# Kernel optimization log

Measured on AMD Instinct MI355X. Metric: run time of the kernel, lower is better.

Reference implementation:

```python
import jax, jax.numpy as jnp
import numpy as np

B, BEAM, TMAX, V, D, H, NL, S, DFF = 4, 5, 16, 50257, 768, 12, 2, 128, 3072
BUF = TMAX + 1  # prefix buffer: sos + TMAX generated tokens
DH = D // H
SOS, EOS = 1, 2
NEG = -1e20


def _ln(x, g, b):
    m = x.mean(-1, keepdims=True)
    v = ((x - m) ** 2).mean(-1, keepdims=True)
    return (x - m) / jnp.sqrt(v + 1e-5) * g + b


def _mha(q_in, kv_in, in_w, in_b, out_w, out_b, bias=None, kpm=None):
    # PyTorch-style MHA: packed in_proj [3D, D], out_proj [D, D]
    q = q_in @ in_w[:D].T + in_b[:D]
    k = kv_in @ in_w[D:2 * D].T + in_b[D:2 * D]
    v = kv_in @ in_w[2 * D:].T + in_b[2 * D:]
    Bq, Tq = q.shape[0], q.shape[1]
    Tk = k.shape[1]
    q = q.reshape(Bq, Tq, H, DH)
    k = k.reshape(Bq, Tk, H, DH)
    v = v.reshape(Bq, Tk, H, DH)
    s = jnp.einsum('bqhd,bkhd->bhqk', q, k) * (1.0 / np.sqrt(DH))
    if bias is not None:
        s = s + bias  # additive causal bias (-10000 * (1 - tril)), as in source
    if kpm is not None:
        s = jnp.where(kpm[:, None, None, :], -1e9, s)  # memory_key_padding_mask
    a = jax.nn.softmax(s, axis=-1)
    o = jnp.einsum('bhqk,bkhd->bqhd', a, v).reshape(Bq, Tq, D)
    return o @ out_w.T + out_b


def _decode(emb, pos, ln_emb_g, ln_emb_b, self_in_w, self_in_b, self_out_w,
            self_out_b, cross_in_w, cross_in_b, cross_out_w, cross_out_b,
            ff1_w, ff1_b, ff2_w, ff2_b, ln1_g, ln1_b, ln2_g, ln2_b, ln3_g,
            ln3_b, dense_w, dense_b, context, source_mask):
    causal = -10000.0 * (1.0 - jnp.tril(jnp.ones((BUF, BUF), jnp.float32)))
    mem = jnp.repeat(context, BEAM, axis=0)            # [B*BEAM, S, D]
    kpm = jnp.repeat(source_mask == 0, BEAM, axis=0)   # True = pad
    # Beam init: nextYs[0] = [sos, 0, 0, ...]; scores trick makes step-0 pick
    # from beam row 0 only, matching beamLk = wordLk[0] in the source.
    buf0 = jnp.zeros((B, BEAM, BUF), jnp.int32).at[:, 0, 0].set(SOS)
    s0 = jnp.concatenate([jnp.zeros((1,), jnp.float32),
                          jnp.full((BEAM - 1,), NEG, jnp.float32)])
    scores0 = jnp.broadcast_to(s0, (B, BEAM))

    def step(carry, t):
        scores, buf = carry
        # no KV cache: re-run full decoder each step (fixed-size padded buffer;
        # causal mask makes positions <= t identical to running on the prefix)
        x = emb[buf.reshape(B * BEAM, BUF)] + pos[None, :BUF]
        x = _ln(x, ln_emb_g, ln_emb_b)
        for l in range(NL):  # post-norm TransformerDecoderLayer, dropout=eval
            sa = _mha(x, x, self_in_w[l], self_in_b[l], self_out_w[l],
                      self_out_b[l], bias=causal)
            x = _ln(x + sa, ln1_g[l], ln1_b[l])
            ca = _mha(x, mem, cross_in_w[l], cross_in_b[l], cross_out_w[l],
                      cross_out_b[l], kpm=kpm)
            x = _ln(x + ca, ln2_g[l], ln2_b[l])
            ff = jax.nn.relu(x @ ff1_w[l].T + ff1_b[l]) @ ff2_w[l].T + ff2_b[l]
            x = _ln(x + ff, ln3_g[l], ln3_b[l])
        h = jnp.tanh(jnp.take(x, t, axis=1) @ dense_w.T + dense_b)  # last pos
        logp = jax.nn.log_softmax(h @ emb.T, axis=-1).reshape(B, BEAM, V)
        last = jnp.take(buf, t, axis=2)  # previous token per beam
        beamLk = logp + scores[:, :, None]
        beamLk = jnp.where((last == EOS)[:, :, None], NEG, beamLk)
        vals, ids = jax.lax.top_k(beamLk.reshape(B, BEAM * V), BEAM)
        prevK = ids // V
        tok = (ids % V).astype(jnp.int32)
        buf = jnp.take_along_axis(buf, prevK[:, :, None], axis=1)
        buf = buf.at[:, :, t + 1].set(tok)
        return (vals, buf), None

    (scores, buf), _ = jax.lax.scan(step, (scores0, buf0), jnp.arange(TMAX))
    toks = buf[:, :, 1:]                         # backtracked hypotheses
    keep = jnp.cumsum(toks == EOS, axis=-1) == 0  # truncate at eos, pad with 0
    preds = jnp.where(keep, toks, 0)
    return scores, preds


def setup_inputs() -> dict:
    key = jax.random.key(0)
    ks = jax.random.split(key, 12)
    r = lambda k, shape: jax.random.normal(k, shape, jnp.float32) * 0.02
    inp = {}
    inp['emb'] = r(ks[0], (V, D))
    inp['pos'] = r(ks[1], (BUF, D))
    inp['ln_emb_g'] = jnp.ones((D,), jnp.float32)
    inp['ln_emb_b'] = jnp.zeros((D,), jnp.float32)
    inp['self_in_w'] = r(ks[2], (NL, 3 * D, D))
    inp['self_in_b'] = jnp.zeros((NL, 3 * D), jnp.float32)
    inp['self_out_w'] = r(ks[3], (NL, D, D))
    inp['self_out_b'] = jnp.zeros((NL, D), jnp.float32)
    inp['cross_in_w'] = r(ks[4], (NL, 3 * D, D))
    inp['cross_in_b'] = jnp.zeros((NL, 3 * D), jnp.float32)
    inp['cross_out_w'] = r(ks[5], (NL, D, D))
    inp['cross_out_b'] = jnp.zeros((NL, D), jnp.float32)
    inp['ff1_w'] = r(ks[6], (NL, DFF, D))
    inp['ff1_b'] = jnp.zeros((NL, DFF), jnp.float32)
    inp['ff2_w'] = r(ks[7], (NL, D, DFF))
    inp['ff2_b'] = jnp.zeros((NL, D), jnp.float32)
    inp['ln1_g'] = jnp.ones((NL, D), jnp.float32)
    inp['ln1_b'] = jnp.zeros((NL, D), jnp.float32)
    inp['ln2_g'] = jnp.ones((NL, D), jnp.float32)
    inp['ln2_b'] = jnp.zeros((NL, D), jnp.float32)
    inp['ln3_g'] = jnp.ones((NL, D), jnp.float32)
    inp['ln3_b'] = jnp.zeros((NL, D), jnp.float32)
    inp['dense_w'] = r(ks[8], (D, D))
    inp['dense_b'] = jnp.zeros((D,), jnp.float32)
    inp['context'] = jax.random.normal(ks[9], (B, S, D), jnp.float32)
    inp['source_mask'] = jnp.ones((B, S), jnp.int32)
    return inp


def reference(emb, pos, ln_emb_g, ln_emb_b, self_in_w, self_in_b, self_out_w,
              self_out_b, cross_in_w, cross_in_b, cross_out_w, cross_out_b,
              ff1_w, ff1_b, ff2_w, ff2_b, ln1_g, ln1_b, ln2_g, ln2_b, ln3_g,
              ln3_b, dense_w, dense_b, context, source_mask):
    return _decode(emb, pos, ln_emb_g, ln_emb_b, self_in_w, self_in_b,
                   self_out_w, self_out_b, cross_in_w, cross_in_b,
                   cross_out_w, cross_out_b, ff1_w, ff1_b, ff2_w, ff2_b,
                   ln1_g, ln1_b, ln2_g, ln2_b, ln3_g, ln3_b, dense_w,
                   dense_b, context, source_mask)
```

## Files before the change

### kernel.cpp

```cpp
#include <hip/hip_runtime.h>
#include <cfloat>
#include <cmath>

constexpr int kV   = 50257;
constexpr int kVP  = 50432;
constexpr int kD   = 768;
constexpr int NLY  = 2;
constexpr int BB   = 4;
constexpr int BEAM = 5;
constexpr int RR   = BB * BEAM;
constexpr int BUFL = 17;
constexpr int SS   = 128;
constexpr int DFF  = 3072;
constexpr int TMAX = 16;
constexpr int SOS  = 1;
constexpr int EOSt = 2;
constexpr int LB   = (kV + 255) / 256;
#define NEGV (-1e20f)

__device__ inline float wave_sum(float v) {
#pragma unroll
  for (int o = 32; o > 0; o >>= 1) v += __shfl_xor(v, o, 64);
  return v;
}
__device__ inline float wave_max(float v) {
#pragma unroll
  for (int o = 32; o > 0; o >>= 1) v = fmaxf(v, __shfl_xor(v, o, 64));
  return v;
}
__device__ inline bool better(float v1, int i1, float v2, int i2) {
  return v1 > v2 || (v1 == v2 && i1 < i2);
}
__device__ inline void insert5(float* tv, int* ti, float v, int i) {
  if (better(v, i, tv[4], ti[4])) {
    tv[4] = v; ti[4] = i;
#pragma unroll
    for (int s = 4; s > 0; --s)
      if (better(tv[s], ti[s], tv[s - 1], ti[s - 1])) {
        float fv = tv[s]; tv[s] = tv[s - 1]; tv[s - 1] = fv;
        int iv = ti[s]; ti[s] = ti[s - 1]; ti[s - 1] = iv;
      }
  }
}
__device__ inline float sel5f(const float* a, int i) {
  float r = a[0];
  r = (i == 1) ? a[1] : r; r = (i == 2) ? a[2] : r;
  r = (i == 3) ? a[3] : r; r = (i == 4) ? a[4] : r;
  return r;
}
__device__ inline int sel5i(const int* a, int i) {
  int r = a[0];
  r = (i == 1) ? a[1] : r; r = (i == 2) ? a[2] : r;
  r = (i == 3) ? a[3] : r; r = (i == 4) ? a[4] : r;
  return r;
}
__device__ inline void merge5(float* av, int* ai, const float* bv, const int* bi) {
  float cv[5]; int ci[5];
  int ia = 0, ib = 0;
#pragma unroll
  for (int s = 0; s < 5; ++s) {
    float va = sel5f(av, ia); int xa = sel5i(ai, ia);
    float vb = sel5f(bv, ib); int xb = sel5i(bi, ib);
    bool ta = better(va, xa, vb, xb);
    cv[s] = ta ? va : vb; ci[s] = ta ? xa : xb;
    ia += ta ? 1 : 0; ib += ta ? 0 : 1;
  }
#pragma unroll
  for (int s = 0; s < 5; ++s) { av[s] = cv[s]; ai[s] = ci[s]; }
}

__global__ void init_k(int* buf0, float* scores) {
  int tid = threadIdx.x;
  if (tid < RR * BUFL) buf0[tid] = 0;
  __syncthreads();
  if (tid < BB) buf0[tid * BEAM * BUFL] = SOS;
  if (tid < RR) scores[tid] = (tid % BEAM == 0) ? 0.f : NEGV;
}

__global__ void transpose_k(const float* __restrict__ src, float* __restrict__ dst,
                            int R, int C, int ds) {
  __shared__ float tile[32][33];
  const int c0 = blockIdx.x * 32, r0 = blockIdx.y * 32;
  const int lx = threadIdx.x & 31, ly = threadIdx.x >> 5;
#pragma unroll
  for (int j = 0; j < 4; ++j) {
    int r = r0 + ly + j * 8;
    if (r < R && c0 + lx < C) tile[ly + j * 8][lx] = src[(size_t)r * C + c0 + lx];
  }
  __syncthreads();
#pragma unroll
  for (int j = 0; j < 4; ++j) {
    int c = c0 + ly + j * 8;
    if (c < C && r0 + lx < R) dst[(size_t)c * ds + r0 + lx] = tile[lx][ly + j * 8];
  }
}

template<bool WT>
__global__ __launch_bounds__(256) void crosskv_k(
    const float* __restrict__ ctx, const float* __restrict__ Wm0,
    const float* __restrict__ bias0, float* __restrict__ ck, float* __restrict__ cv) {
  const int l = blockIdx.z;
  const float* Wm = Wm0 + (size_t)l * 2304 * 768;
  const float* bias = bias0 + l * 2304;
  __shared__ float a_s[16 * 768];
  __shared__ float ps[4 * 64 * 17];
  const int tid = threadIdx.x;
  const int row0 = blockIdx.y * 16;
  for (int i = tid * 4; i < 16 * 768; i += 1024) {
    int rr = i / 768, k = i - rr * 768;
    *(float4*)&a_s[i] = *(const float4*)&ctx[(size_t)(row0 + rr) * 768 + k];
  }
  __syncthreads();
  const int w = tid >> 6, lane = tid & 63;
  const int colg = 768 + blockIdx.x * 64 + lane;
  const int kb = w * 192;
  float acc[16];
#pragma unroll
  for (int r = 0; r < 16; ++r) acc[r] = 0.f;
  for (int k4 = 0; k4 < 48; ++k4) {
    const int k = kb + k4 * 4;
    float w0, w1, w2, w3;
    if (WT) {
      w0 = Wm[(size_t)(k + 0) * 2304 + colg]; w1 = Wm[(size_t)(k + 1) * 2304 + colg];
      w2 = Wm[(size_t)(k + 2) * 2304 + colg]; w3 = Wm[(size_t)(k + 3) * 2304 + colg];
    } else {
      float4 wv = *(const float4*)&Wm[(size_t)colg * 768 + k];
      w0 = wv.x; w1 = wv.y; w2 = wv.z; w3 = wv.w;
    }
#pragma unroll
    for (int r = 0; r < 16; ++r) {
      float4 a = *(const float4*)&a_s[r * 768 + k];
      acc[r] = fmaf(a.x, w0, fmaf(a.y, w1, fmaf(a.z, w2, fmaf(a.w, w3, acc[r]))));
    }
  }
#pragma unroll
  for (int r = 0; r < 16; ++r) ps[(w * 64 + lane) * 17 + r] = acc[r];
  __syncthreads();
  for (int o = tid; o < 1024; o += 256) {
    int rr = o >> 6, cl = o & 63;
    int cg = 768 + blockIdx.x * 64 + cl;
    float v = bias[cg];
#pragma unroll
    for (int ww = 0; ww < 4; ++ww) v += ps[(ww * 64 + cl) * 17 + rr];
    int gr = row0 + rr;
    int b = gr >> 7, s = gr & 127;
    int c = cg - 768, kv = c / 768, n = c - kv * 768;
    float* dst = kv ? cv : ck;
    dst[((size_t)(l * 4 + b) * 128 + s) * 768 + n] = v;
  }
}

template<bool WT>
__global__ __launch_bounds__(256) void gemm20_k(
    const float* __restrict__ Wm, int wstride, const float* __restrict__ bias, int N,
    int pre, const float* __restrict__ xsrc, const float* __restrict__ tmp_in,
    const float* __restrict__ lng, const float* __restrict__ lnb, float* __restrict__ xout,
    int outmode, float* __restrict__ out0,
    float* __restrict__ kcl, float* __restrict__ vcl, int t,
    const float* __restrict__ embp, const float* __restrict__ posw, const int* __restrict__ bufn,
    int reorder_t, const float* __restrict__ kco, const float* __restrict__ vco,
    float* __restrict__ kcn, float* __restrict__ vcn, const int* __restrict__ prevK) {
  __shared__ float a_s[RR * 768];
  __shared__ float ps[4 * 64 * 21];
  __shared__ float mS[RR], rS[RR];
  __shared__ int tokS[RR];
  const int tid = threadIdx.x;

  if (reorder_t > 0) {
    const int per = 768 * reorder_t;
    const int tot = 2 * RR * per;
    for (int i = blockIdx.x * 256 + tid; i < tot; i += gridDim.x * 256) {
      int half = i / (RR * per);
      int rem = i - half * RR * per;
      int r = rem / per;
      int rem2 = rem - r * per;
      int p = rem2 / 768;
      int d = rem2 - p * 768;
      int src = (r / BEAM) * BEAM + prevK[r];
      if (half == 0) kcn[(r * BUFL + p) * 768 + d] = kco[(src * BUFL + p) * 768 + d];
      else           vcn[(r * BUFL + p) * 768 + d] = vco[(src * BUFL + p) * 768 + d];
    }
  }
  if (pre == 1 && tid < RR) tokS[tid] = bufn[tid * BUFL + t];
  __syncthreads();
  for (int i = tid * 4; i < RR * 768; i += 1024) {
    int r = i / 768, k = i - r * 768;
    float4 v;
    if (pre == 0) v = *(const float4*)&xsrc[i];
    else if (pre == 1) {
      float4 e = *(const float4*)&embp[(size_t)tokS[r] * 768 + k];
      float4 p = *(const float4*)&posw[(size_t)t * 768 + k];
      v = make_float4(e.x + p.x, e.y + p.y, e.z + p.z, e.w + p.w);
    } else {
      float4 a = *(const float4*)&xsrc[i];
      float4 b = *(const float4*)&tmp_in[i];
      v = make_float4(a.x + b.x, a.y + b.y, a.z + b.z, a.w + b.w);
    }
    *(float4*)&a_s[i] = v;
  }
  __syncthreads();
  if (pre != 0) {
    const int w0 = tid >> 6, ln = tid & 63;
    for (int r = w0 * 5; r < w0 * 5 + 5; ++r) {
      float s = 0.f, q = 0.f;
      for (int k = ln; k < 768; k += 64) { float v = a_s[r * 768 + k]; s += v; q += v * v; }
      s = wave_sum(s); q = wave_sum(q);
      if (ln == 0) {
        float m = s / 768.f;
        float var = q / 768.f - m * m;
        mS[r] = m; rS[r] = 1.f / sqrtf(var + 1e-5f);
      }
    }
    __syncthreads();
    for (int i = tid * 4; i < RR * 768; i += 1024) {
      int r = i / 768, k = i - r * 768;
      float4 v = *(const float4*)&a_s[i];
      float4 g = *(const float4*)&lng[k];
      float4 b = *(const float4*)&lnb[k];
      float m = mS[r], rs = rS[r];
      v = make_float4((v.x - m) * rs * g.x + b.x, (v.y - m) * rs * g.y + b.y,
                      (v.z - m) * rs * g.z + b.z, (v.w - m) * rs * g.w + b.w);
      *(float4*)&a_s[i] = v;
    }
    __syncthreads();
    if (xout != nullptr && blockIdx.x == 0) {
      for (int i = tid * 4; i < RR * 768; i += 1024)
        *(float4*)&xout[i] = *(const float4*)&a_s[i];
    }
  }
  const int w = tid >> 6, lane = tid & 63;
  const int colg = blockIdx.x * 64 + lane;
  const int kb = w * 192;
  float acc[RR];
#pragma unroll
  for (int r = 0; r < RR; ++r) acc[r] = 0.f;
  for (int k4 = 0; k4 < 48; ++k4) {
    const int k = kb + k4 * 4;
    float w0, w1, w2, w3;
    if (WT) {
      w0 = Wm[(size_t)(k + 0) * wstride + colg]; w1 = Wm[(size_t)(k + 1) * wstride + colg];
      w2 = Wm[(size_t)(k + 2) * wstride + colg]; w3 = Wm[(size_t)(k + 3) * wstride + colg];
    } else {
      float4 wv = *(const float4*)&Wm[(size_t)colg * 768 + k];
      w0 = wv.x; w1 = wv.y; w2 = wv.z; w3 = wv.w;
    }
#pragma unroll
    for (int r = 0; r < RR; ++r) {
      float4 a = *(const float4*)&a_s[r * 768 + k];
      acc[r] = fmaf(a.x, w0, fmaf(a.y, w1, fmaf(a.z, w2, fmaf(a.w, w3, acc[r]))));
    }
  }
#pragma unroll
  for (int r = 0; r < RR; ++r) ps[(w * 64 + lane) * 21 + r] = acc[r];
  __syncthreads();
  for (int o = tid; o < RR * 64; o += 256) {
    int r = o >> 6, cl = o & 63;
    int cg = blockIdx.x * 64 + cl;
    float v = bias[cg];
#pragma unroll
    for (int ww = 0; ww < 4; ++ww) v += ps[(ww * 64 + cl) * 21 + r];
    if (outmode == 1) v = fmaxf(v, 0.f);
    else if (outmode == 2) v = tanhf(v);
    if (outmode == 3) {
      if (cg < 768) out0[r * 768 + cg];
      if (cg < 768) out0[r * 768 + cg] = v;
      else if (cg < 1536) kcl[(r * BUFL + t) * 768 + (cg - 768)] = v;
      else vcl[(r * BUFL + t) * 768 + (cg - 1536)] = v;
    } else {
      out0[(size_t)r * N + cg] = v;
    }
  }
}

template<bool WT>
__global__ __launch_bounds__(1024) void ff2_k(
    const float* __restrict__ Wm, const float* __restrict__ bias,
    const float* __restrict__ A, float* __restrict__ out0) {
  __shared__ float ps[64 * 16 * 21];
  const int tid = threadIdx.x;
  const int w = tid >> 6, lane = tid & 63;
  const int cl = lane & 15, ksub = lane >> 4;
  const int colg = blockIdx.x * 16 + cl;
  const int kb = w * 192 + ksub * 48;
  float acc[RR];
#pragma unroll
  for (int r = 0; r < RR; ++r) acc[r] = 0.f;
  for (int k4 = 0; k4 < 12; ++k4) {
    const int k = kb + k4 * 4;
    float w0, w1, w2, w3;
    if (WT) {
      w0 = Wm[(size_t)(k + 0) * 768 + colg]; w1 = Wm[(size_t)(k + 1) * 768 + colg];
      w2 = Wm[(size_t)(k + 2) * 768 + colg]; w3 = Wm[(size_t)(k + 3) * 768 + colg];
    } else {
      float4 wv = *(const float4*)&Wm[(size_t)colg * 3072 + k];
      w0 = wv.x; w1 = wv.y; w2 = wv.z; w3 = wv.w;
    }
#pragma unroll
    for (int r = 0; r < RR; ++r) {
      float4 a = *(const float4*)&A[r * 3072 + k];
      acc[r] = fmaf(a.x, w0, fmaf(a.y, w1, fmaf(a.z, w2, fmaf(a.w, w3, acc[r]))));
    }
  }
  const int seg = w * 4 + ksub;
#pragma unroll
  for (int r = 0; r < RR; ++r) ps[(seg * 16 + cl) * 21 + r] = acc[r];
  __syncthreads();
  if (tid < RR * 16) {
    int r = tid >> 4, c2 = tid & 15;
    float v = bias[blockIdx.x * 16 + c2];
    for (int s2 = 0; s2 < 64; ++s2) v += ps[(s2 * 16 + c2) * 21 + r];
    out0[r * 768 + blockIdx.x * 16 + c2] = v;
  }
}

__global__ __launch_bounds__(64) void self_attn_k(
    const float* __restrict__ qb, const float* __restrict__ kcn,
    const float* __restrict__ vcn, float* __restrict__ outb, int t) {
  const int r = blockIdx.x, hh = blockIdx.y, lane = threadIdx.x;
  __shared__ float qs[64];
  __shared__ float ks[16 * 65];
  __shared__ float pp[16];
  qs[lane] = qb[r * 768 + hh * 64 + lane];
  for (int p = 0; p <= t; ++p)
    ks[p * 65 + lane] = kcn[(r * BUFL + p) * 768 + hh * 64 + lane];
  __syncthreads();
  float s = -1e30f;
  if (lane <= t) {
    float a = 0.f;
#pragma unroll
    for (int d = 0; d < 64; ++d) a = fmaf(qs[d], ks[lane * 65 + d], a);
    s = a * 0.125f;
  }
  float m = wave_max(s);
  float p = expf(s - m);
  float sum = wave_sum(p);
  if (lane <= t) pp[lane] = p / sum;
  __syncthreads();
  const float* vb = vcn + r * BUFL * 768 + hh * 64 + lane;
  float o = 0.f;
  for (int k = 0; k <= t; ++k) o = fmaf(pp[k], vb[k * 768], o);
  outb[r * 768 + hh * 64 + lane] = o;
}

__global__ __launch_bounds__(64) void cross_attn_k(
    const float* __restrict__ qb, const float* __restrict__ ck,
    const float* __restrict__ cv, const int* __restrict__ smask,
    float* __restrict__ outb) {
  const int r = blockIdx.x, hh = blockIdx.y, lane = threadIdx.x;
  const int b = r / BEAM;
  __shared__ float qs[64];
  __shared__ float ks[128 * 65];
  __shared__ float pp[128];
  qs[lane] = qb[r * 768 + hh * 64 + lane];
  for (int p = 0; p < 128; ++p)
    ks[p * 65 + lane] = ck[((size_t)b * 128 + p) * 768 + hh * 64 + lane];
  __syncthreads();
  float a0 = 0.f, a1 = 0.f;
#pragma unroll
  for (int d = 0; d < 64; ++d) {
    a0 = fmaf(qs[d], ks[lane * 65 + d], a0);
    a1 = fmaf(qs[d], ks[(lane + 64) * 65 + d], a1);
  }
  float s0 = a0 * 0.125f, s1 = a1 * 0.125f;
  if (smask[b * 128 + lane] == 0)      s0 = -1e9f;
  if (smask[b * 128 + lane + 64] == 0) s1 = -1e9f;
  float m = wave_max(fmaxf(s0, s1));
  float p0 = expf(s0 - m), p1 = expf(s1 - m);
  float sum = wave_sum(p0 + p1);
  pp[lane] = p0 / sum; pp[lane + 64] = p1 / sum;
  __syncthreads();
  const float* vb = cv + (size_t)b * 128 * 768 + hh * 64 + lane;
  float o0 = 0.f, o1 = 0.f, o2 = 0.f, o3 = 0.f;
  for (int k = 0; k < 128; k += 4) {
    o0 = fmaf(pp[k + 0], vb[(k + 0) * 768], o0);
    o1 = fmaf(pp[k + 1], vb[(k + 1) * 768], o1);
    o2 = fmaf(pp[k + 2], vb[(k + 2) * 768], o2);
    o3 = fmaf(pp[k + 3], vb[(k + 3) * 768], o3);
  }
  outb[r * 768 + hh * 64 + lane] = (o0 + o1) + (o2 + o3);
}

template<bool ET>
__global__ __launch_bounds__(256) void logits_k(
    const float* __restrict__ hbuf, const float* __restrict__ embM,
    float* __restrict__ candV, int* __restrict__ candI,
    float* __restrict__ mrow, float* __restrict__ srow) {
  __shared__ float hs[RR * 768];
  __shared__ float vv[4 * 256];
  const int tid = threadIdx.x, blk = blockIdx.x;
  for (int i = tid * 4; i < RR * 768; i += 1024)
    *(float4*)&hs[i] = *(const float4*)&hbuf[i];
  __syncthreads();
  const int col = blk * 256 + tid;
  const bool valid = col < kV;
  const int colc = valid ? col : (kV - 1);
  float acc[RR];
#pragma unroll
  for (int r = 0; r < RR; ++r) acc[r] = 0.f;
  for (int k = 0; k < 768; k += 4) {
    float w0, w1, w2, w3;
    if (ET) {
      w0 = embM[(size_t)(k + 0) * kVP + col]; w1 = embM[(size_t)(k + 1) * kVP + col];
      w2 = embM[(size_t)(k + 2) * kVP + col]; w3 = embM[(size_t)(k + 3) * kVP + col];
    } else {
      float4 wv = *(const float4*)&embM[(size_t)colc * 768 + k];
      w0 = wv.x; w1 = wv.y; w2 = wv.z; w3 = wv.w;
    }
#pragma unroll
    for (int r = 0; r < RR; ++r) {
      float4 a = *(const float4*)&hs[r * 768 + k];
      acc[r] = fmaf(a.x, w0, fmaf(a.y, w1, fmaf(a.z, w2, fmaf(a.w, w3, acc[r]))));
    }
  }
  const int w = tid >> 6, lane = tid & 63;
  for (int g = 0; g < 5; ++g) {
#pragma unroll
    for (int j = 0; j < 4; ++j) vv[j * 256 + tid] = valid ? acc[g * 4 + j] : -FLT_MAX;
    __syncthreads();
    const int r = g * 4 + w;
    float v[4]; int gc[4]; bool used[4];
#pragma unroll
    for (int j = 0; j < 4; ++j) {
      v[j] = vv[w * 256 + lane * 4 + j];
      gc[j] = blk * 256 + lane * 4 + j;
      used[j] = false;
    }
    float tv[5]; int tg[5];
#pragma unroll
    for (int round = 0; round < 5; ++round) {
      float bv = -FLT_MAX; int bidx = 0x7fffffff; int bj = -1;
#pragma unroll
      for (int j = 0; j < 4; ++j) {
        bool c = (!used[j]) && better(v[j], gc[j], bv, bidx);
        bv = c ? v[j] : bv; bidx = c ? gc[j] : bidx; bj = c ? j : bj;
      }
      float wv2 = bv; int wi = bidx;
      for (int d = 1; d < 64; d <<= 1) {
        float ov = __shfl_xor(wv2, d, 64); int oi = __shfl_xor(wi, d, 64);
        if (better(ov, oi, wv2, wi)) { wv2 = ov; wi = oi; }
      }
      tv[round] = wv2; tg[round] = wi;
      if (bj >= 0 && bidx == wi) used[bj] = true;
    }
    float m = tv[0];
    float s = 0.f;
#pragma unroll
    for (int j = 0; j < 4; ++j) s += expf(v[j] - m);
    s = wave_sum(s);
    if (lane == 0) {
      mrow[r * LB + blk] = m;
      srow[r * LB + blk] = s;
#pragma unroll
      for (int q = 0; q < 5; ++q) {
        candV[(r * LB + blk) * 5 + q] = tv[q];
        candI[(r * LB + blk) * 5 + q] = tg[q];
      }
    }
    __syncthreads();
  }
}

__global__ __launch_bounds__(256) void topk_k(
    const float* __restrict__ candV, const int* __restrict__ candI,
    const float* __restrict__ mrow, const float* __restrict__ srow,
    float* __restrict__ scores, const int* __restrict__ bufc, int* __restrict__ bufn,
    int t, int* __restrict__ prevK, int* __restrict__ tokv) {
  const int b = blockIdx.x, tid = threadIdx.x;
  const int w = tid >> 6, lane = tid & 63;
  __shared__ float lseS[5], scS[5];
  __shared__ int emS[5];
  __shared__ float wv5[4][5]; __shared__ int wi5[4][5];
  __shared__ int fpk[5], ftok[5];
  for (int j = w; j < 5; j += 4) {
    const int gr = b * 5 + j;
    float M = -FLT_MAX, S = 0.f;
    for (int e = lane; e < LB; e += 64) {
      float m2 = mrow[gr * LB + e], s2 = srow[gr * LB + e];
      if (m2 > M) { S = S * expf(M - m2) + s2; M = m2; }
      else        { S += s2 * expf(m2 - M); }
    }
    for (int d = 1; d < 64; d <<= 1) {
      float Mo = __shfl_xor(M, d, 64), So = __shfl_xor(S, d, 64);
      float Mn = fmaxf(M, Mo);
      S = S * expf(M - Mn) + So * expf(Mo - Mn);
      M = Mn;
    }
    if (lane == 0) {
      lseS[j] = M + logf(S);
      scS[j] = scores[gr];
      emS[j] = (bufc[gr * BUFL + t] == EOSt);
    }
  }
  __syncthreads();
  float tv[5]; int ti[5];
#pragma unroll
  for (int s = 0; s < 5; ++s) { tv[s] = -FLT_MAX; ti[s] = 0x7fffffff; }
  for (int i = tid; i < 5 * LB * 5; i += 256) {
    int j = i / (LB * 5);
    int e = i - j * LB * 5;
    int blk = e / 5, rk = e - blk * 5;
    int gr = b * 5 + j;
    float cvv = candV[(gr * LB + blk) * 5 + rk];
    int col = candI[(gr * LB + blk) * 5 + rk];
    float val = emS[j] ? NEGV : (cvv - lseS[j] + scS[j]);
    insert5(tv, ti, val, j * kV + col);
  }
  for (int d = 1; d < 64; d <<= 1) {
    float ov[5]; int oi[5];
#pragma unroll
    for (int s = 0; s < 5; ++s) { ov[s] = __shfl_xor(tv[s], d, 64); oi[s] = __shfl_xor(ti[s], d, 64); }
    merge5(tv, ti, ov, oi);
  }
  if (lane == 0) {
#pragma unroll
    for (int s = 0; s < 5; ++s) { wv5[w][s] = tv[s]; wi5[w][s] = ti[s]; }
  }
  __syncthreads();
  if (tid == 0) {
    float av[5]; int ai[5];
#pragma unroll
    for (int s = 0; s < 5; ++s) { av[s] = wv5[0][s]; ai[s] = wi5[0][s]; }
    for (int ww = 1; ww < 4; ++ww) {
      float bv[5]; int bi[5];
#pragma unroll
      for (int s = 0; s < 5; ++s) { bv[s] = wv5[ww][s]; bi[s] = wi5[ww][s]; }
      merge5(av, ai, bv, bi);
    }
#pragma unroll
    for (int s = 0; s < 5; ++s) {
      int pk = ai[s] / kV;
      int tk = ai[s] - pk * kV;
      scores[b * 5 + s] = av[s];
      prevK[b * 5 + s] = pk; tokv[b * 5 + s] = tk;
      fpk[s] = pk; ftok[s] = tk;
    }
  }
  __syncthreads();
  for (int i = tid; i < 5 * BUFL; i += 256) {
    int j = i / BUFL, p = i - j * BUFL;
    int src = b * 5 + fpk[j];
    int val = (p == t + 1) ? ftok[j] : bufc[src * BUFL + p];
    bufn[(b * 5 + j) * BUFL + p] = val;
  }
}

__global__ void finalize_k(const float* __restrict__ scores, const int* __restrict__ buf,
                           float* __restrict__ out) {
  const int tid = threadIdx.x;
  if (tid < RR) {
    out[tid] = scores[tid];
    int seen = 0;
    for (int i = 0; i < TMAX; ++i) {
      int tk = buf[tid * BUFL + 1 + i];
      if (tk == EOSt) seen = 1;
      out[RR + tid * TMAX + i] = seen ? 0.f : (float)tk;
    }
  }
}

extern "C" void kernel_launch(void* const* d_in, const int* in_sizes, int n_in,
                              void* d_out, int out_size, void* d_ws, size_t ws_size,
                              hipStream_t stream) {
  const float* emb        = (const float*)d_in[0];
  const float* pos        = (const float*)d_in[1];
  const float* ln_emb_g   = (const float*)d_in[2];
  const float* ln_emb_b   = (const float*)d_in[3];
  const float* self_in_w  = (const float*)d_in[4];
  const float* self_in_b  = (const float*)d_in[5];
  const float* self_out_w = (const float*)d_in[6];
  const float* self_out_b = (const float*)d_in[7];
  const float* cross_in_w = (const float*)d_in[8];
  const float* cross_in_b = (const float*)d_in[9];
  const float* cross_out_w= (const float*)d_in[10];
  const float* cross_out_b= (const float*)d_in[11];
  const float* ff1_w      = (const float*)d_in[12];
  const float* ff1_b      = (const float*)d_in[13];
  const float* ff2_w      = (const float*)d_in[14];
  const float* ff2_b      = (const float*)d_in[15];
  const float* ln1_g      = (const float*)d_in[16];
  const float* ln1_b      = (const float*)d_in[17];
  const float* ln2_g      = (const float*)d_in[18];
  const float* ln2_b      = (const float*)d_in[19];
  const float* ln3_g      = (const float*)d_in[20];
  const float* ln3_b      = (const float*)d_in[21];
  const float* dense_w    = (const float*)d_in[22];
  const float* dense_b    = (const float*)d_in[23];
  const float* context    = (const float*)d_in[24];
  const int*   source_mask= (const int*)d_in[25];

  float* wsf = (float*)d_ws;
  size_t off = 0;
  auto alloc = [&](size_t n) { float* p = wsf + off; off += (n + 3) & ~(size_t)3; return p; };

  float* XA    = alloc(RR * 768);
  float* XB    = alloc(RR * 768);
  float* XC    = alloc(RR * 768);
  float* qb    = alloc(RR * 768);
  float* attnb = alloc(RR * 768);
  float* tmp   = alloc(RR * 768);
  float* hbuf  = alloc(RR * 768);
  float* ffb   = alloc(RR * 3072);
  float* candV = alloc(RR * LB * 5);
  float* mrow  = alloc(RR * LB);
  float* srow  = alloc(RR * LB);
  float* scores= alloc(32);
  float* ck    = alloc((size_t)NLY * 4 * 128 * 768);
  float* cv    = alloc((size_t)NLY * 4 * 128 * 768);
  const size_t cacheSeg = (size_t)RR * BUFL * 768;
  float* kcB   = alloc(4 * cacheSeg);
  float* vcB   = alloc(4 * cacheSeg);
  int* candI   = (int*)alloc(RR * LB * 5);
  int* bufs0   = (int*)alloc(RR * BUFL + 12);
  int* bufs1   = (int*)alloc(RR * BUFL + 12);
  int* prevKp  = (int*)alloc(32);
  int* tokp    = (int*)alloc(32);
  const size_t baseFloats = off;

  const size_t nSiT = (size_t)768 * 2304, nSoT = (size_t)768 * 768;
  const size_t nCiT = nSiT, nCoT = nSoT, nF1T = (size_t)768 * 3072, nF2T = (size_t)3072 * 768;
  const size_t wtFloats = 2 * (nSiT + nSoT + nCiT + nCoT + nF1T + nF2T) + nSoT;
  const size_t embTFloats = (size_t)768 * kVP;
  const bool useWT = ws_size >= (baseFloats + wtFloats) * 4;
  const bool useET = useWT && ws_size >= (baseFloats + wtFloats + embTFloats) * 4;

  float* siT[2]; float* soT[2]; float* ciT[2]; float* coT[2]; float* f1T[2]; float* f2T[2];
  float* dT = nullptr; float* embT = nullptr;
  if (useWT) {
    for (int l = 0; l < 2; ++l) siT[l] = alloc(nSiT);
    for (int l = 0; l < 2; ++l) soT[l] = alloc(nSoT);
    for (int l = 0; l < 2; ++l) ciT[l] = alloc(nCiT);
    for (int l = 0; l < 2; ++l) coT[l] = alloc(nCoT);
    for (int l = 0; l < 2; ++l) f1T[l] = alloc(nF1T);
    for (int l = 0; l < 2; ++l) f2T[l] = alloc(nF2T);
    dT = alloc(nSoT);
    if (useET) embT = alloc(embTFloats);
  }

  init_k<<<1, 512, 0, stream>>>(bufs0, scores);

  if (useWT) {
    auto T = [&](const float* src, float* dst, int R, int C, int ds) {
      dim3 g((C + 31) / 32, (R + 31) / 32);
      transpose_k<<<g, 256, 0, stream>>>(src, dst, R, C, ds);
    };
    for (int l = 0; l < 2; ++l) {
      T(self_in_w  + (size_t)l * 2304 * 768, siT[l], 2304, 768, 2304);
      T(self_out_w + (size_t)l * 768 * 768,  soT[l], 768, 768, 768);
      T(cross_in_w + (size_t)l * 2304 * 768, ciT[l], 2304, 768, 2304);
      T(cross_out_w+ (size_t)l * 768 * 768,  coT[l], 768, 768, 768);
      T(ff1_w      + (size_t)l * 3072 * 768, f1T[l], 3072, 768, 3072);
      T(ff2_w      + (size_t)l * 768 * 3072, f2T[l], 768, 3072, 768);
    }
    T(dense_w, dT, 768, 768, 768);
    if (useET) T(emb, embT, kV, 768, kVP);
  }

  {
    dim3 g(24, 32, 2);
    if (useWT) crosskv_k<true><<<g, 256, 0, stream>>>(context, ciT[0], cross_in_b, ck, cv);
    else       crosskv_k<false><<<g, 256, 0, stream>>>(context, cross_in_w, cross_in_b, ck, cv);
  }

  const int* bc = bufs0;
  auto G = [&](const float* Wt, const float* Wg, int wstride,
               const float* bias, int N, int pre, const float* xsrc, const float* tmpin,
               const float* g2, const float* b2, float* xout, int outmode, float* out0,
               float* kcl, float* vcl, int tt,
               int reorder_t, const float* kco, const float* vco, float* kcn2, float* vcn2) {
    dim3 grid(N / 64);
    if (useWT)
      gemm20_k<true><<<grid, 256, 0, stream>>>(Wt, wstride, bias, N, pre, xsrc, tmpin, g2, b2,
        xout, outmode, out0, kcl, vcl, tt, emb, pos, bc, reorder_t, kco, vco, kcn2, vcn2, prevKp);
    else
      gemm20_k<false><<<grid, 256, 0, stream>>>(Wg, wstride, bias, N, pre, xsrc, tmpin, g2, b2,
        xout, outmode, out0, kcl, vcl, tt, emb, pos, bc, reorder_t, kco, vco, kcn2, vcn2, prevKp);
  };

  for (int t = 0; t < TMAX; ++t) {
    bc = (t & 1) ? bufs1 : bufs0;
    int* bn = (t & 1) ? bufs0 : bufs1;
    const int np = (t + 1) & 1, op = t & 1;

    for (int l = 0; l < 2; ++l) {
      float* kNew = kcB + (np * 2 + l) * cacheSeg;
      float* vNew = vcB + (np * 2 + l) * cacheSeg;
      float* kOld = kcB + (op * 2 + l) * cacheSeg;
      float* vOld = vcB + (op * 2 + l) * cacheSeg;
      if (l == 0)
        G(siT[0], self_in_w, 2304, self_in_b, 2304,
          1, nullptr, nullptr, ln_emb_g, ln_emb_b, XA,
          3, qb, kNew, vNew, t, t, kOld, vOld, kNew, vNew);
      else
        G(siT[1], self_in_w + (size_t)2304 * 768, 2304, self_in_b + 2304, 2304,
          2, XC, tmp, ln3_g, ln3_b, XA,
          3, qb, kNew, vNew, t, t, kOld, vOld, kNew, vNew);
      self_attn_k<<<dim3(RR, 12), 64, 0, stream>>>(qb, kNew, vNew, attnb, t);
      G(soT[l], self_out_w + (size_t)l * 768 * 768, 768, self_out_b + l * 768, 768,
        0, attnb, nullptr, nullptr, nullptr, nullptr, 0, tmp,
        nullptr, nullptr, t, 0, nullptr, nullptr, nullptr, nullptr);
      G(ciT[l], cross_in_w + (size_t)l * 2304 * 768, 2304, cross_in_b + l * 2304, 768,
        2, XA, tmp, ln1_g + l * 768, ln1_b + l * 768, XB, 0, qb,
        nullptr, nullptr, t, 0, nullptr, nullptr, nullptr, nullptr);
      cross_attn_k<<<dim3(RR, 12), 64, 0, stream>>>(
          qb, ck + (size_t)l * 4 * 128 * 768, cv + (size_t)l * 4 * 128 * 768, source_mask, attnb);
      G(coT[l], cross_out_w + (size_t)l * 768 * 768, 768, cross_out_b + l * 768, 768,
        0, attnb, nullptr, nullptr, nullptr, nullptr, 0, tmp,
        nullptr, nullptr, t, 0, nullptr, nullptr, nullptr, nullptr);
      G(f1T[l], ff1_w + (size_t)l * 3072 * 768, 3072, ff1_b + l * 3072, 3072,
        2, XB, tmp, ln2_g + l * 768, ln2_b + l * 768, XC, 1, ffb,
        nullptr, nullptr, t, 0, nullptr, nullptr, nullptr, nullptr);
      if (useWT) ff2_k<true><<<48, 1024, 0, stream>>>(f2T[l], ff2_b + l * 768, ffb, tmp);
      else       ff2_k<false><<<48, 1024, 0, stream>>>(ff2_w + (size_t)l * 768 * 3072, ff2_b + l * 768, ffb, tmp);
    }
    G(dT, dense_w, 768, dense_b, 768,
      2, XC, tmp, ln3_g + 768, ln3_b + 768, nullptr, 2, hbuf,
      nullptr, nullptr, t, 0, nullptr, nullptr, nullptr, nullptr);
    if (useET) logits_k<true><<<LB, 256, 0, stream>>>(hbuf, embT, candV, candI, mrow, srow);
    else       logits_k<false><<<LB, 256, 0, stream>>>(hbuf, emb, candV, candI, mrow, srow);
    topk_k<<<BB, 256, 0, stream>>>(candV, candI, mrow, srow, scores, bc, bn, t, prevKp, tokp);
  }

  finalize_k<<<1, 64, 0, stream>>>(scores, bufs0, (float*)d_out);
}
```

Measured before the change: 11.21 ms.

## Fuse decode loop into one persistent kernel with software grid barriers

Replaces the per-step launches of GEMM, attention, FF2, logits and top-k kernels with a single persistent kernel of 256 blocks. Stages are separated by an atomic-counter grid barrier. FF2 is split along K into partial sums that the next stage reduces, together with the bias and residual. KV-cache reordering moves into its own vectorized stage. This removes roughly a hundred kernel launches per decode, but it relies on all 256 blocks being co-resident. It also leaves most blocks idle during small stages such as the 12-block GEMMs.

Result: slower. 18.79 ms (+67.6%).

```diff
diff --git a/kernel.cpp b/kernel.cpp
--- a/kernel.cpp
+++ b/kernel.cpp
@@ -16,7 +16,11 @@
 constexpr int SOS  = 1;
 constexpr int EOSt = 2;
 constexpr int LB   = (kV + 255) / 256;
+constexpr int NBLK = 256;
+constexpr size_t CSEG = (size_t)RR * BUFL * 768;
 #define NEGV (-1e20f)
+
+static_assert(RR * 768 == 15360, "A-tile size");
 
 __device__ inline float wave_sum(float v) {
 #pragma unroll
@@ -68,9 +72,31 @@
 #pragma unroll
   for (int s = 0; s < 5; ++s) { av[s] = cv[s]; ai[s] = ci[s]; }
 }
-
-__global__ void init_k(int* buf0, float* scores) {
+__device__ inline float4 f4add(float4 a, float4 b) {
+  return make_float4(a.x + b.x, a.y + b.y, a.z + b.z, a.w + b.w);
+}
+
+__device__ __forceinline__ void grid_sync(int* bar) {
+  __syncthreads();
+  if (threadIdx.x == 0) {
+    int* cnt = bar; int* gen = bar + 1;
+    const int g = __hip_atomic_load(gen, __ATOMIC_RELAXED, __HIP_MEMORY_SCOPE_AGENT);
+    const int prev = __hip_atomic_fetch_add(cnt, 1, __ATOMIC_ACQ_REL, __HIP_MEMORY_SCOPE_AGENT);
+    if (prev == NBLK - 1) {
+      __hip_atomic_store(cnt, 0, __ATOMIC_RELAXED, __HIP_MEMORY_SCOPE_AGENT);
+      __hip_atomic_fetch_add(gen, 1, __ATOMIC_RELEASE, __HIP_MEMORY_SCOPE_AGENT);
+    } else {
+      while (__hip_atomic_load(gen, __ATOMIC_RELAXED, __HIP_MEMORY_SCOPE_AGENT) == g)
+        __builtin_amdgcn_s_sleep(2);
+      __builtin_amdgcn_fence(__ATOMIC_ACQUIRE, "agent");
+    }
+  }
+  __syncthreads();
+}
+
+__global__ void init_k(int* buf0, float* scores, int* bar) {
   int tid = threadIdx.x;
+  if (tid < 16) bar[tid] = 0;
   if (tid < RR * BUFL) buf0[tid] = 0;
   __syncthreads();
   if (tid < BB) buf0[tid * BEAM * BUFL] = SOS;
@@ -150,86 +176,75 @@
   }
 }
 
+
 template<bool WT>
-__global__ __launch_bounds__(256) void gemm20_k(
+__device__ void gemm_stage(int vb, float* UN,
     const float* __restrict__ Wm, int wstride, const float* __restrict__ bias, int N,
     int pre, const float* __restrict__ xsrc, const float* __restrict__ tmp_in,
-    const float* __restrict__ lng, const float* __restrict__ lnb, float* __restrict__ xout,
-    int outmode, float* __restrict__ out0,
+    const float* __restrict__ lng, const float* __restrict__ lnb,
+    float* __restrict__ xout, int outmode, float* __restrict__ out0,
     float* __restrict__ kcl, float* __restrict__ vcl, int t,
-    const float* __restrict__ embp, const float* __restrict__ posw, const int* __restrict__ bufn,
-    int reorder_t, const float* __restrict__ kco, const float* __restrict__ vco,
-    float* __restrict__ kcn, float* __restrict__ vcn, const int* __restrict__ prevK) {
-  __shared__ float a_s[RR * 768];
-  __shared__ float ps[4 * 64 * 21];
+    const float* __restrict__ embp, const float* __restrict__ posw,
+    const int* __restrict__ bufn,
+    const float* __restrict__ pf, const float* __restrict__ bias2) {
   __shared__ float mS[RR], rS[RR];
   __shared__ int tokS[RR];
   const int tid = threadIdx.x;
-
-  if (reorder_t > 0) {
-    const int per = 768 * reorder_t;
-    const int tot = 2 * RR * per;
-    for (int i = blockIdx.x * 256 + tid; i < tot; i += gridDim.x * 256) {
-      int half = i / (RR * per);
-      int rem = i - half * RR * per;
-      int r = rem / per;
-      int rem2 = rem - r * per;
-      int p = rem2 / 768;
-      int d = rem2 - p * 768;
-      int src = (r / BEAM) * BEAM + prevK[r];
-      if (half == 0) kcn[(r * BUFL + p) * 768 + d] = kco[(src * BUFL + p) * 768 + d];
-      else           vcn[(r * BUFL + p) * 768 + d] = vco[(src * BUFL + p) * 768 + d];
-    }
-  }
+  float* a_s = UN;
   if (pre == 1 && tid < RR) tokS[tid] = bufn[tid * BUFL + t];
   __syncthreads();
   for (int i = tid * 4; i < RR * 768; i += 1024) {
-    int r = i / 768, k = i - r * 768;
+    const int r = i / 768, k = i - r * 768;
     float4 v;
-    if (pre == 0) v = *(const float4*)&xsrc[i];
-    else if (pre == 1) {
-      float4 e = *(const float4*)&embp[(size_t)tokS[r] * 768 + k];
-      float4 p = *(const float4*)&posw[(size_t)t * 768 + k];
-      v = make_float4(e.x + p.x, e.y + p.y, e.z + p.z, e.w + p.w);
+    if (pre == 0) {
+      v = *(const float4*)&xsrc[i];
+    } else if (pre == 1) {
+      const float4 e = *(const float4*)&embp[(size_t)tokS[r] * 768 + k];
+      const float4 pz = *(const float4*)&posw[(size_t)t * 768 + k];
+      v = f4add(e, pz);
+    } else if (pre == 2) {
+      v = f4add(*(const float4*)&xsrc[i], *(const float4*)&tmp_in[i]);
     } else {
-      float4 a = *(const float4*)&xsrc[i];
-      float4 b = *(const float4*)&tmp_in[i];
-      v = make_float4(a.x + b.x, a.y + b.y, a.z + b.z, a.w + b.w);
+      float4 v0 = f4add(*(const float4*)&xsrc[i], *(const float4*)&bias2[k]);
+      v0 = f4add(v0, *(const float4*)&pf[i]);
+      v0 = f4add(v0, *(const float4*)&pf[15360 + i]);
+      v0 = f4add(v0, *(const float4*)&pf[30720 + i]);
+      v = f4add(v0, *(const float4*)&pf[46080 + i]);
     }
     *(float4*)&a_s[i] = v;
   }
   __syncthreads();
   if (pre != 0) {
-    const int w0 = tid >> 6, ln = tid & 63;
-    for (int r = w0 * 5; r < w0 * 5 + 5; ++r) {
+    const int wq = tid >> 6, ln = tid & 63;
+    for (int r = wq * 5; r < wq * 5 + 5; ++r) {
       float s = 0.f, q = 0.f;
-      for (int k = ln; k < 768; k += 64) { float v = a_s[r * 768 + k]; s += v; q += v * v; }
+      for (int k = ln; k < 768; k += 64) { const float v = a_s[r * 768 + k]; s += v; q += v * v; }
       s = wave_sum(s); q = wave_sum(q);
       if (ln == 0) {
-        float m = s / 768.f;
-        float var = q / 768.f - m * m;
+        const float m = s / 768.f;
+        const float var = q / 768.f - m * m;
         mS[r] = m; rS[r] = 1.f / sqrtf(var + 1e-5f);
       }
     }
     __syncthreads();
     for (int i = tid * 4; i < RR * 768; i += 1024) {
-      int r = i / 768, k = i - r * 768;
+      const int r = i / 768, k = i - r * 768;
       float4 v = *(const float4*)&a_s[i];
-      float4 g = *(const float4*)&lng[k];
-      float4 b = *(const float4*)&lnb[k];
-      float m = mS[r], rs = rS[r];
+      const float4 g = *(const float4*)&lng[k];
+      const float4 b = *(const float4*)&lnb[k];
+      const float m = mS[r], rs = rS[r];
       v = make_float4((v.x - m) * rs * g.x + b.x, (v.y - m) * rs * g.y + b.y,
                       (v.z - m) * rs * g.z + b.z, (v.w - m) * rs * g.w + b.w);
       *(float4*)&a_s[i] = v;
     }
     __syncthreads();
-    if (xout != nullptr && blockIdx.x == 0) {
+    if (xout != nullptr && vb == 0) {
       for (int i = tid * 4; i < RR * 768; i += 1024)
         *(float4*)&xout[i] = *(const float4*)&a_s[i];
     }
   }
   const int w = tid >> 6, lane = tid & 63;
-  const int colg = blockIdx.x * 64 + lane;
+  const int colg = vb * 64 + lane;
   const int kb = w * 192;
   float acc[RR];
 #pragma unroll
@@ -238,31 +253,34 @@
     const int k = kb + k4 * 4;
     float w0, w1, w2, w3;
     if (WT) {
-      w0 = Wm[(size_t)(k + 0) * wstride + colg]; w1 = Wm[(size_t)(k + 1) * wstride + colg];
-      w2 = Wm[(size_t)(k + 2) * wstride + colg]; w3 = Wm[(size_t)(k + 3) * wstride + colg];
+      w0 = Wm[(size_t)(k + 0) * wstride + colg];
+      w1 = Wm[(size_t)(k + 1) * wstride + colg];
+      w2 = Wm[(size_t)(k + 2) * wstride + colg];
+      w3 = Wm[(size_t)(k + 3) * wstride + colg];
     } else {
-      float4 wv = *(const float4*)&Wm[(size_t)colg * 768 + k];
+      const float4 wv = *(const float4*)&Wm[(size_t)colg * 768 + k];
       w0 = wv.x; w1 = wv.y; w2 = wv.z; w3 = wv.w;
     }
 #pragma unroll
     for (int r = 0; r < RR; ++r) {
-      float4 a = *(const float4*)&a_s[r * 768 + k];
+      const float4 a = *(const float4*)&a_s[r * 768 + k];
       acc[r] = fmaf(a.x, w0, fmaf(a.y, w1, fmaf(a.z, w2, fmaf(a.w, w3, acc[r]))));
     }
   }
+  __syncthreads();
+  float* ps = UN;
 #pragma unroll
   for (int r = 0; r < RR; ++r) ps[(w * 64 + lane) * 21 + r] = acc[r];
   __syncthreads();
   for (int o = tid; o < RR * 64; o += 256) {
-    int r = o >> 6, cl = o & 63;
-    int cg = blockIdx.x * 64 + cl;
+    const int r = o >> 6, cl = o & 63;
+    const int cg = vb * 64 + cl;
     float v = bias[cg];
 #pragma unroll
     for (int ww = 0; ww < 4; ++ww) v += ps[(ww * 64 + cl) * 21 + r];
     if (outmode == 1) v = fmaxf(v, 0.f);
     else if (outmode == 2) v = tanhf(v);
     if (outmode == 3) {
-      if (cg < 768) out0[r * 768 + cg];
       if (cg < 768) out0[r * 768 + cg] = v;
       else if (cg < 1536) kcl[(r * BUFL + t) * 768 + (cg - 768)] = v;
       else vcl[(r * BUFL + t) * 768 + (cg - 1536)] = v;
@@ -272,16 +290,115 @@
   }
 }
 
+__device__ void reorder_stage(int vb, int nb, int t,
+    const float* __restrict__ kco, const float* __restrict__ vco,
+    float* __restrict__ kcn, float* __restrict__ vcn, const int* __restrict__ prevK) {
+  const int per = 192 * t;
+  const int tot = 2 * RR * per;
+  for (int i = vb * 256 + (int)threadIdx.x; i < tot; i += nb * 256) {
+    const int half = i / (RR * per);
+    int rem = i - half * RR * per;
+    const int r = rem / per;
+    rem -= r * per;
+    const int p2 = rem / 192;
+    const int d4 = (rem - p2 * 192) * 4;
+    const int src = (r / BEAM) * BEAM + prevK[r];
+    if (half == 0)
+      *(float4*)&kcn[(r * BUFL + p2) * 768 + d4] = *(const float4*)&kco[(src * BUFL + p2) * 768 + d4];
+    else
+      *(float4*)&vcn[(r * BUFL + p2) * 768 + d4] = *(const float4*)&vco[(src * BUFL + p2) * 768 + d4];
+  }
+}
+
+__device__ void self_attn_stage(int vb, float* UN, const float* __restrict__ qb,
+    const float* __restrict__ kcn, const float* __restrict__ vcn,
+    float* __restrict__ outb, int t) {
+  __shared__ float qs[64];
+  __shared__ float pp[16];
+  const int tid = threadIdx.x, w = tid >> 6, lane = tid & 63;
+  const int r = vb % RR, hh = vb / RR;
+  float* ks = UN;
+  if (w == 0) qs[lane] = qb[r * 768 + hh * 64 + lane];
+  for (int p2 = w; p2 <= t; p2 += 4)
+    ks[p2 * 65 + lane] = kcn[(r * BUFL + p2) * 768 + hh * 64 + lane];
+  __syncthreads();
+  if (w == 0) {
+    float s = -1e30f;
+    if (lane <= t) {
+      float a = 0.f;
+#pragma unroll
+      for (int d = 0; d < 64; ++d) a = fmaf(qs[d], ks[lane * 65 + d], a);
+      s = a * 0.125f;
+    }
+    const float m = wave_max(s);
+    const float pex = expf(s - m);
+    const float sum = wave_sum(pex);
+    if (lane <= t) pp[lane] = pex / sum;
+  }
+  __syncthreads();
+  if (w == 0) {
+    const float* vbp = vcn + r * BUFL * 768 + hh * 64 + lane;
+    float o = 0.f;
+    for (int k = 0; k <= t; ++k) o = fmaf(pp[k], vbp[k * 768], o);
+    outb[r * 768 + hh * 64 + lane] = o;
+  }
+}
+
+__device__ void cross_attn_stage(int vb, float* UN, const float* __restrict__ qb,
+    const float* __restrict__ ck, const float* __restrict__ cv,
+    const int* __restrict__ smask, float* __restrict__ outb) {
+  __shared__ float qs[64];
+  __shared__ float pp[128];
+  __shared__ float vpart[4 * 64];
+  const int tid = threadIdx.x, w = tid >> 6, lane = tid & 63;
+  const int r = vb % RR, hh = vb / RR, b = r / BEAM;
+  float* ks = UN;
+  if (w == 0) qs[lane] = qb[r * 768 + hh * 64 + lane];
+  for (int p2 = w; p2 < 128; p2 += 4)
+    ks[p2 * 65 + lane] = ck[((size_t)b * 128 + p2) * 768 + hh * 64 + lane];
+  __syncthreads();
+  if (w == 0) {
+    float a0 = 0.f, a1 = 0.f;
+#pragma unroll
+    for (int d = 0; d < 64; ++d) {
+      a0 = fmaf(qs[d], ks[lane * 65 + d], a0);
+      a1 = fmaf(qs[d], ks[(lane + 64) * 65 + d], a1);
+    }
+    float s0 = a0 * 0.125f, s1 = a1 * 0.125f;
+    if (smask[b * 128 + lane] == 0)      s0 = -1e9f;
+    if (smask[b * 128 + lane + 64] == 0) s1 = -1e9f;
+    const float m = wave_max(fmaxf(s0, s1));
+    const float p0 = expf(s0 - m), p1 = expf(s1 - m);
+    const float sum = wave_sum(p0 + p1);
+    pp[lane] = p0 / sum; pp[lane + 64] = p1 / sum;
+  }
+  __syncthreads();
+  {
+    const float* vbp = cv + (size_t)b * 128 * 768 + hh * 64 + lane;
+    float o0 = 0.f, o1 = 0.f, o2 = 0.f, o3 = 0.f;
+    for (int k = w * 32; k < w * 32 + 32; k += 4) {
+      o0 = fmaf(pp[k + 0], vbp[(k + 0) * 768], o0);
+      o1 = fmaf(pp[k + 1], vbp[(k + 1) * 768], o1);
+      o2 = fmaf(pp[k + 2], vbp[(k + 2) * 768], o2);
+      o3 = fmaf(pp[k + 3], vbp[(k + 3) * 768], o3);
+    }
+    vpart[w * 64 + lane] = (o0 + o1) + (o2 + o3);
+  }
+  __syncthreads();
+  if (w == 0)
+    outb[r * 768 + hh * 64 + lane] =
+        (vpart[lane] + vpart[64 + lane]) + (vpart[128 + lane] + vpart[192 + lane]);
+}
+
 template<bool WT>
-__global__ __launch_bounds__(1024) void ff2_k(
-    const float* __restrict__ Wm, const float* __restrict__ bias,
-    const float* __restrict__ A, float* __restrict__ out0) {
-  __shared__ float ps[64 * 16 * 21];
-  const int tid = threadIdx.x;
-  const int w = tid >> 6, lane = tid & 63;
+__device__ void ff2A_stage(int vb, float* UN, const float* __restrict__ Wm,
+                           const float* __restrict__ A, float* __restrict__ pf) {
+  float* ps = UN;
+  const int tid = threadIdx.x, w = tid >> 6, lane = tid & 63;
   const int cl = lane & 15, ksub = lane >> 4;
-  const int colg = blockIdx.x * 16 + cl;
-  const int kb = w * 192 + ksub * 48;
+  const int kt = vb / 48, ct = vb - kt * 48;
+  const int colg = ct * 16 + cl;
+  const int kb = kt * 768 + w * 192 + ksub * 48;
   float acc[RR];
 #pragma unroll
   for (int r = 0; r < RR; ++r) acc[r] = 0.f;
@@ -289,15 +406,17 @@
     const int k = kb + k4 * 4;
     float w0, w1, w2, w3;
     if (WT) {
-      w0 = Wm[(size_t)(k + 0) * 768 + colg]; w1 = Wm[(size_t)(k + 1) * 768 + colg];
-      w2 = Wm[(size_t)(k + 2) * 768 + colg]; w3 = Wm[(size_t)(k + 3) * 768 + colg];
+      w0 = Wm[(size_t)(k + 0) * 768 + colg];
+      w1 = Wm[(size_t)(k + 1) * 768 + colg];
+      w2 = Wm[(size_t)(k + 2) * 768 + colg];
+      w3 = Wm[(size_t)(k + 3) * 768 + colg];
     } else {
-      float4 wv = *(const float4*)&Wm[(size_t)colg * 3072 + k];
+      const float4 wv = *(const float4*)&Wm[(size_t)colg * 3072 + k];
       w0 = wv.x; w1 = wv.y; w2 = wv.z; w3 = wv.w;
     }
 #pragma unroll
     for (int r = 0; r < RR; ++r) {
-      float4 a = *(const float4*)&A[r * 3072 + k];
+      const float4 a = *(const float4*)&A[r * 3072 + k];
       acc[r] = fmaf(a.x, w0, fmaf(a.y, w1, fmaf(a.z, w2, fmaf(a.w, w3, acc[r]))));
     }
   }
@@ -305,89 +424,23 @@
 #pragma unroll
   for (int r = 0; r < RR; ++r) ps[(seg * 16 + cl) * 21 + r] = acc[r];
   __syncthreads();
-  if (tid < RR * 16) {
-    int r = tid >> 4, c2 = tid & 15;
-    float v = bias[blockIdx.x * 16 + c2];
-    for (int s2 = 0; s2 < 64; ++s2) v += ps[(s2 * 16 + c2) * 21 + r];
-    out0[r * 768 + blockIdx.x * 16 + c2] = v;
-  }
-}
-
-__global__ __launch_bounds__(64) void self_attn_k(
-    const float* __restrict__ qb, const float* __restrict__ kcn,
-    const float* __restrict__ vcn, float* __restrict__ outb, int t) {
-  const int r = blockIdx.x, hh = blockIdx.y, lane = threadIdx.x;
-  __shared__ float qs[64];
-  __shared__ float ks[16 * 65];
-  __shared__ float pp[16];
-  qs[lane] = qb[r * 768 + hh * 64 + lane];
-  for (int p = 0; p <= t; ++p)
-    ks[p * 65 + lane] = kcn[(r * BUFL + p) * 768 + hh * 64 + lane];
-  __syncthreads();
-  float s = -1e30f;
-  if (lane <= t) {
-    float a = 0.f;
-#pragma unroll
-    for (int d = 0; d < 64; ++d) a = fmaf(qs[d], ks[lane * 65 + d], a);
-    s = a * 0.125f;
-  }
-  float m = wave_max(s);
-  float p = expf(s - m);
-  float sum = wave_sum(p);
-  if (lane <= t) pp[lane] = p / sum;
-  __syncthreads();
-  const float* vb = vcn + r * BUFL * 768 + hh * 64 + lane;
-  float o = 0.f;
-  for (int k = 0; k <= t; ++k) o = fmaf(pp[k], vb[k * 768], o);
-  outb[r * 768 + hh * 64 + lane] = o;
-}
-
-__global__ __launch_bounds__(64) void cross_attn_k(
-    const float* __restrict__ qb, const float* __restrict__ ck,
-    const float* __restrict__ cv, const int* __restrict__ smask,
-    float* __restrict__ outb) {
-  const int r = blockIdx.x, hh = blockIdx.y, lane = threadIdx.x;
-  const int b = r / BEAM;
-  __shared__ float qs[64];
-  __shared__ float ks[128 * 65];
-  __shared__ float pp[128];
-  qs[lane] = qb[r * 768 + hh * 64 + lane];
-  for (int p = 0; p < 128; ++p)
-    ks[p * 65 + lane] = ck[((size_t)b * 128 + p) * 768 + hh * 64 + lane];
-  __syncthreads();
-  float a0 = 0.f, a1 = 0.f;
-#pragma unroll
-  for (int d = 0; d < 64; ++d) {
-    a0 = fmaf(qs[d], ks[lane * 65 + d], a0);
-    a1 = fmaf(qs[d], ks[(lane + 64) * 65 + d], a1);
-  }
-  float s0 = a0 * 0.125f, s1 = a1 * 0.125f;
-  if (smask[b * 128 + lane] == 0)      s0 = -1e9f;
-  if (smask[b * 128 + lane + 64] == 0) s1 = -1e9f;
-  float m = wave_max(fmaxf(s0, s1));
-  float p0 = expf(s0 - m), p1 = expf(s1 - m);
-  float sum = wave_sum(p0 + p1);
-  pp[lane] = p0 / sum; pp[lane + 64] = p1 / sum;
-  __syncthreads();
-  const float* vb = cv + (size_t)b * 128 * 768 + hh * 64 + lane;
-  float o0 = 0.f, o1 = 0.f, o2 = 0.f, o3 = 0.f;
-  for (int k = 0; k < 128; k += 4) {
-    o0 = fmaf(pp[k + 0], vb[(k + 0) * 768], o0);
-    o1 = fmaf(pp[k + 1], vb[(k + 1) * 768], o1);
-    o2 = fmaf(pp[k + 2], vb[(k + 2) * 768], o2);
-    o3 = fmaf(pp[k + 3], vb[(k + 3) * 768], o3);
-  }
-  outb[r * 768 + hh * 64 + lane] = (o0 + o1) + (o2 + o3);
+  for (int o = tid; o < RR * 16; o += 256) {
+    const int r = o >> 4, c2 = o & 15;
+    float v = 0.f;
+#pragma unroll
+    for (int s2 = 0; s2 < 16; ++s2) v += ps[(s2 * 16 + c2) * 21 + r];
+    pf[kt * 15360 + r * 768 + ct * 16 + c2] = v;
+  }
 }
 
 template<bool ET>
-__global__ __launch_bounds__(256) void logits_k(
+__device__ void logits_stage(int blk, float* UN,
     const float* __restrict__ hbuf, const float* __restrict__ embM,
     float* __restrict__ candV, int* __restrict__ candI,
     float* __restrict__ mrow, float* __restrict__ srow) {
-  __shared__ float hs[RR * 768];
   __shared__ float vv[4 * 256];
-  const int tid = threadIdx.x, blk = blockIdx.x;
+  float* hs = UN;
+  const int tid = threadIdx.x;
   for (int i = tid * 4; i < RR * 768; i += 1024)
     *(float4*)&hs[i] = *(const float4*)&hbuf[i];
   __syncthreads();
@@ -400,15 +453,17 @@
   for (int k = 0; k < 768; k += 4) {
     float w0, w1, w2, w3;
     if (ET) {
-      w0 = embM[(size_t)(k + 0) * kVP + col]; w1 = embM[(size_t)(k + 1) * kVP + col];
-      w2 = embM[(size_t)(k + 2) * kVP + col]; w3 = embM[(size_t)(k + 3) * kVP + col];
+      w0 = embM[(size_t)(k + 0) * kVP + col];
+      w1 = embM[(size_t)(k + 1) * kVP + col];
+      w2 = embM[(size_t)(k + 2) * kVP + col];
+      w3 = embM[(size_t)(k + 3) * kVP + col];
     } else {
-      float4 wv = *(const float4*)&embM[(size_t)colc * 768 + k];
+      const float4 wv = *(const float4*)&embM[(size_t)colc * 768 + k];
       w0 = wv.x; w1 = wv.y; w2 = wv.z; w3 = wv.w;
     }
 #pragma unroll
     for (int r = 0; r < RR; ++r) {
-      float4 a = *(const float4*)&hs[r * 768 + k];
+      const float4 a = *(const float4*)&hs[r * 768 + k];
       acc[r] = fmaf(a.x, w0, fmaf(a.y, w1, fmaf(a.z, w2, fmaf(a.w, w3, acc[r]))));
     }
   }
@@ -431,18 +486,18 @@
       float bv = -FLT_MAX; int bidx = 0x7fffffff; int bj = -1;
 #pragma unroll
       for (int j = 0; j < 4; ++j) {
-        bool c = (!used[j]) && better(v[j], gc[j], bv, bidx);
+        const bool c = (!used[j]) && better(v[j], gc[j], bv, bidx);
         bv = c ? v[j] : bv; bidx = c ? gc[j] : bidx; bj = c ? j : bj;
       }
       float wv2 = bv; int wi = bidx;
       for (int d = 1; d < 64; d <<= 1) {
-        float ov = __shfl_xor(wv2, d, 64); int oi = __shfl_xor(wi, d, 64);
+        const float ov = __shfl_xor(wv2, d, 64); const int oi = __shfl_xor(wi, d, 64);
         if (better(ov, oi, wv2, wi)) { wv2 = ov; wi = oi; }
       }
       tv[round] = wv2; tg[round] = wi;
       if (bj >= 0 && bidx == wi) used[bj] = true;
     }
-    float m = tv[0];
+    const float m = tv[0];
     float s = 0.f;
 #pragma unroll
     for (int j = 0; j < 4; ++j) s += expf(v[j] - m);
@@ -460,12 +515,11 @@
   }
 }
 
-__global__ __launch_bounds__(256) void topk_k(
-    const float* __restrict__ candV, const int* __restrict__ candI,
+__device__ void topk_stage(int b, const float* __restrict__ candV, const int* __restrict__ candI,
     const float* __restrict__ mrow, const float* __restrict__ srow,
     float* __restrict__ scores, const int* __restrict__ bufc, int* __restrict__ bufn,
     int t, int* __restrict__ prevK, int* __restrict__ tokv) {
-  const int b = blockIdx.x, tid = threadIdx.x;
+  const int tid = threadIdx.x;
   const int w = tid >> 6, lane = tid & 63;
   __shared__ float lseS[5], scS[5];
   __shared__ int emS[5];
@@ -475,13 +529,13 @@
     const int gr = b * 5 + j;
     float M = -FLT_MAX, S = 0.f;
     for (int e = lane; e < LB; e += 64) {
-      float m2 = mrow[gr * LB + e], s2 = srow[gr * LB + e];
+      const float m2 = mrow[gr * LB + e], s2 = srow[gr * LB + e];
       if (m2 > M) { S = S * expf(M - m2) + s2; M = m2; }
       else        { S += s2 * expf(m2 - M); }
     }
     for (int d = 1; d < 64; d <<= 1) {
-      float Mo = __shfl_xor(M, d, 64), So = __shfl_xor(S, d, 64);
-      float Mn = fmaxf(M, Mo);
+      const float Mo = __shfl_xor(M, d, 64), So = __shfl_xor(S, d, 64);
+      const float Mn = fmaxf(M, Mo);
       S = S * expf(M - Mn) + So * expf(Mo - Mn);
       M = Mn;
     }
@@ -496,13 +550,13 @@
 #pragma unroll
   for (int s = 0; s < 5; ++s) { tv[s] = -FLT_MAX; ti[s] = 0x7fffffff; }
   for (int i = tid; i < 5 * LB * 5; i += 256) {
-    int j = i / (LB * 5);
-    int e = i - j * LB * 5;
-    int blk = e / 5, rk = e - blk * 5;
-    int gr = b * 5 + j;
-    float cvv = candV[(gr * LB + blk) * 5 + rk];
-    int col = candI[(gr * LB + blk) * 5 + rk];
-    float val = emS[j] ? NEGV : (cvv - lseS[j] + scS[j]);
+    const int j = i / (LB * 5);
+    const int e = i - j * (LB * 5);
+    const int blk = e / 5, rk = e - blk * 5;
+    const int gr = b * 5 + j;
+    const float cvv = candV[(gr * LB + blk) * 5 + rk];
+    const int col = candI[(gr * LB + blk) * 5 + rk];
+    const float val = emS[j] ? NEGV : (cvv - lseS[j] + scS[j]);
     insert5(tv, ti, val, j * kV + col);
   }
   for (int d = 1; d < 64; d <<= 1) {
@@ -528,8 +582,8 @@
     }
 #pragma unroll
     for (int s = 0; s < 5; ++s) {
-      int pk = ai[s] / kV;
-      int tk = ai[s] - pk * kV;
+      const int pk = ai[s] / kV;
+      const int tk = ai[s] - pk * kV;
       scores[b * 5 + s] = av[s];
       prevK[b * 5 + s] = pk; tokv[b * 5 + s] = tk;
       fpk[s] = pk; ftok[s] = tk;
@@ -537,23 +591,113 @@
   }
   __syncthreads();
   for (int i = tid; i < 5 * BUFL; i += 256) {
-    int j = i / BUFL, p = i - j * BUFL;
-    int src = b * 5 + fpk[j];
-    int val = (p == t + 1) ? ftok[j] : bufc[src * BUFL + p];
-    bufn[(b * 5 + j) * BUFL + p] = val;
-  }
-}
-
-__global__ void finalize_k(const float* __restrict__ scores, const int* __restrict__ buf,
-                           float* __restrict__ out) {
-  const int tid = threadIdx.x;
-  if (tid < RR) {
-    out[tid] = scores[tid];
-    int seen = 0;
-    for (int i = 0; i < TMAX; ++i) {
-      int tk = buf[tid * BUFL + 1 + i];
-      if (tk == EOSt) seen = 1;
-      out[RR + tid * TMAX + i] = seen ? 0.f : (float)tk;
+    const int j = i / BUFL, p2 = i - j * BUFL;
+    const int src = b * 5 + fpk[j];
+    const int val = (p2 == t + 1) ? ftok[j] : bufc[src * BUFL + p2];
+    bufn[(b * 5 + j) * BUFL + p2] = val;
+  }
+}
+
+struct DecP {
+  const float *emb, *pos, *ln_emb_g, *ln_emb_b;
+  const float *self_in_b, *self_out_b, *cross_in_b, *cross_out_b;
+  const float *ff1_b, *ff2_b, *dense_b;
+  const float *ln1_g, *ln1_b, *ln2_g, *ln2_b, *ln3_g, *ln3_b;
+  const int* smask;
+  const float *Wqkv0, *Wqkv1, *Wso0, *Wso1, *Wcq0, *Wcq1, *Wco0, *Wco1;
+  const float *Wf10, *Wf11, *Wf20, *Wf21, *Wd, *embM;
+  float *XA, *XB, *XC, *qb, *attnb, *tmp, *hbuf, *ffb, *pf;
+  float *candV, *mrow, *srow, *scores;
+  float *ck, *cv, *kcB, *vcB;
+  int *candI, *bufs0, *bufs1, *prevK, *tok;
+  int* bar;
+  float* out;
+};
+
+template<bool WT, bool ET>
+__global__ __launch_bounds__(256) void decode_k(DecP p) {
+  __shared__ float UN[15360];
+  const int vb = blockIdx.x;
+#pragma unroll 1
+  for (int t = 0; t < TMAX; ++t) {
+    const int* bc = (t & 1) ? p.bufs1 : p.bufs0;
+    int* bn = (t & 1) ? p.bufs0 : p.bufs1;
+    const int np = (t + 1) & 1, op = t & 1;
+#pragma unroll 1
+    for (int l = 0; l < 2; ++l) {
+      float* kNew = p.kcB + (size_t)(np * 2 + l) * CSEG;
+      float* vNew = p.vcB + (size_t)(np * 2 + l) * CSEG;
+      const float* kOld = p.kcB + (size_t)(op * 2 + l) * CSEG;
+      const float* vOld = p.vcB + (size_t)(op * 2 + l) * CSEG;
+      if (vb < 36) {
+        if (l == 0)
+          gemm_stage<WT>(vb, UN, p.Wqkv0, 2304, p.self_in_b, 2304,
+                         1, nullptr, nullptr, p.ln_emb_g, p.ln_emb_b, p.XA,
+                         3, p.qb, kNew, vNew, t, p.emb, p.pos, bc, nullptr, nullptr);
+        else
+          gemm_stage<WT>(vb, UN, p.Wqkv1, 2304, p.self_in_b + 2304, 2304,
+                         3, p.XC, nullptr, p.ln3_g, p.ln3_b, p.XA,
+                         3, p.qb, kNew, vNew, t, nullptr, nullptr, nullptr,
+                         p.pf, p.ff2_b);
+      } else if (t > 0) {
+        reorder_stage(vb - 36, NBLK - 36, t, kOld, vOld, kNew, vNew, p.prevK);
+      }
+      grid_sync(p.bar);
+      if (vb < RR * 12) self_attn_stage(vb, UN, p.qb, kNew, vNew, p.attnb, t);
+      grid_sync(p.bar);
+      if (vb < 12)
+        gemm_stage<WT>(vb, UN, l ? p.Wso1 : p.Wso0, 768, p.self_out_b + l * 768, 768,
+                       0, p.attnb, nullptr, nullptr, nullptr, nullptr,
+                       0, p.tmp, nullptr, nullptr, t,
+                       nullptr, nullptr, nullptr, nullptr, nullptr);
+      grid_sync(p.bar);
+      if (vb < 12)
+        gemm_stage<WT>(vb, UN, l ? p.Wcq1 : p.Wcq0, 2304, p.cross_in_b + l * 2304, 768,
+                       2, p.XA, p.tmp, p.ln1_g + l * 768, p.ln1_b + l * 768, p.XB,
+                       0, p.qb, nullptr, nullptr, t,
+                       nullptr, nullptr, nullptr, nullptr, nullptr);
+      grid_sync(p.bar);
+      if (vb < RR * 12)
+        cross_attn_stage(vb, UN, p.qb,
+                         p.ck + (size_t)l * 4 * 128 * 768,
+                         p.cv + (size_t)l * 4 * 128 * 768, p.smask, p.attnb);
+      grid_sync(p.bar);
+      if (vb < 12)
+        gemm_stage<WT>(vb, UN, l ? p.Wco1 : p.Wco0, 768, p.cross_out_b + l * 768, 768,
+                       0, p.attnb, nullptr, nullptr, nullptr, nullptr,
+                       0, p.tmp, nullptr, nullptr, t,
+                       nullptr, nullptr, nullptr, nullptr, nullptr);
+      grid_sync(p.bar);
+      if (vb < 48)
+        gemm_stage<WT>(vb, UN, l ? p.Wf11 : p.Wf10, 3072, p.ff1_b + l * 3072, 3072,
+                       2, p.XB, p.tmp, p.ln2_g + l * 768, p.ln2_b + l * 768, p.XC,
+                       1, p.ffb, nullptr, nullptr, t,
+                       nullptr, nullptr, nullptr, nullptr, nullptr);
+      grid_sync(p.bar);
+      if (vb < 192) ff2A_stage<WT>(vb, UN, l ? p.Wf21 : p.Wf20, p.ffb, p.pf);
+      grid_sync(p.bar);
+    }
+    if (vb < 12)
+      gemm_stage<WT>(vb, UN, p.Wd, 768, p.dense_b, 768,
+                     3, p.XC, nullptr, p.ln3_g + 768, p.ln3_b + 768, nullptr,
+                     2, p.hbuf, nullptr, nullptr, t,
+                     nullptr, nullptr, nullptr, p.pf, p.ff2_b + 768);
+    grid_sync(p.bar);
+    if (vb < LB) logits_stage<ET>(vb, UN, p.hbuf, p.embM, p.candV, p.candI, p.mrow, p.srow);
+    grid_sync(p.bar);
+    if (vb < BB) topk_stage(vb, p.candV, p.candI, p.mrow, p.srow, p.scores, bc, bn, t, p.prevK, p.tok);
+    grid_sync(p.bar);
+  }
+  if (vb == 0) {
+    const int tid = threadIdx.x;
+    if (tid < RR) {
+      p.out[tid] = p.scores[tid];
+      int seen = 0;
+      for (int i = 0; i < TMAX; ++i) {
+        const int tk = p.bufs0[tid * BUFL + 1 + i];
+        if (tk == EOSt) seen = 1;
+        p.out[RR + tid * TMAX + i] = seen ? 0.f : (float)tk;
+      }
     }
   }
 }
@@ -606,14 +750,15 @@
   float* scores= alloc(32);
   float* ck    = alloc((size_t)NLY * 4 * 128 * 768);
   float* cv    = alloc((size_t)NLY * 4 * 128 * 768);
-  const size_t cacheSeg = (size_t)RR * BUFL * 768;
-  float* kcB   = alloc(4 * cacheSeg);
-  float* vcB   = alloc(4 * cacheSeg);
+  float* kcB   = alloc(4 * CSEG);
+  float* vcB   = alloc(4 * CSEG);
+  float* pf    = alloc(4 * RR * 768);
   int* candI   = (int*)alloc(RR * LB * 5);
   int* bufs0   = (int*)alloc(RR * BUFL + 12);
   int* bufs1   = (int*)alloc(RR * BUFL + 12);
   int* prevKp  = (int*)alloc(32);
   int* tokp    = (int*)alloc(32);
+  int* bar     = (int*)alloc(16);
   const size_t baseFloats = off;
 
   const size_t nSiT = (size_t)768 * 2304, nSoT = (size_t)768 * 768;
@@ -636,7 +781,7 @@
     if (useET) embT = alloc(embTFloats);
   }
 
-  init_k<<<1, 512, 0, stream>>>(bufs0, scores);
+  init_k<<<1, 512, 0, stream>>>(bufs0, scores, bar);
 
   if (useWT) {
     auto T = [&](const float* src, float* dst, int R, int C, int ds) {
@@ -661,64 +806,36 @@
     else       crosskv_k<false><<<g, 256, 0, stream>>>(context, cross_in_w, cross_in_b, ck, cv);
   }
 
-  const int* bc = bufs0;
-  auto G = [&](const float* Wt, const float* Wg, int wstride,
-               const float* bias, int N, int pre, const float* xsrc, const float* tmpin,
-               const float* g2, const float* b2, float* xout, int outmode, float* out0,
-               float* kcl, float* vcl, int tt,
-               int reorder_t, const float* kco, const float* vco, float* kcn2, float* vcn2) {
-    dim3 grid(N / 64);
-    if (useWT)
-      gemm20_k<true><<<grid, 256, 0, stream>>>(Wt, wstride, bias, N, pre, xsrc, tmpin, g2, b2,
-        xout, outmode, out0, kcl, vcl, tt, emb, pos, bc, reorder_t, kco, vco, kcn2, vcn2, prevKp);
-    else
-      gemm20_k<false><<<grid, 256, 0, stream>>>(Wg, wstride, bias, N, pre, xsrc, tmpin, g2, b2,
-        xout, outmode, out0, kcl, vcl, tt, emb, pos, bc, reorder_t, kco, vco, kcn2, vcn2, prevKp);
-  };
-
-  for (int t = 0; t < TMAX; ++t) {
-    bc = (t & 1) ? bufs1 : bufs0;
-    int* bn = (t & 1) ? bufs0 : bufs1;
-    const int np = (t + 1) & 1, op = t & 1;
-
-    for (int l = 0; l < 2; ++l) {
-      float* kNew = kcB + (np * 2 + l) * cacheSeg;
-      float* vNew = vcB + (np * 2 + l) * cacheSeg;
-      float* kOld = kcB + (op * 2 + l) * cacheSeg;
-      float* vOld = vcB + (op * 2 + l) * cacheSeg;
-      if (l == 0)
-        G(siT[0], self_in_w, 2304, self_in_b, 2304,
-          1, nullptr, nullptr, ln_emb_g, ln_emb_b, XA,
-          3, qb, kNew, vNew, t, t, kOld, vOld, kNew, vNew);
-      else
-        G(siT[1], self_in_w + (size_t)2304 * 768, 2304, self_in_b + 2304, 2304,
-          2, XC, tmp, ln3_g, ln3_b, XA,
-          3, qb, kNew, vNew, t, t, kOld, vOld, kNew, vNew);
-      self_attn_k<<<dim3(RR, 12), 64, 0, stream>>>(qb, kNew, vNew, attnb, t);
-      G(soT[l], self_out_w + (size_t)l * 768 * 768, 768, self_out_b + l * 768, 768,
-        0, attnb, nullptr, nullptr, nullptr, nullptr, 0, tmp,
-        nullptr, nullptr, t, 0, nullptr, nullptr, nullptr, nullptr);
-      G(ciT[l], cross_in_w + (size_t)l * 2304 * 768, 2304, cross_in_b + l * 2304, 768,
-        2, XA, tmp, ln1_g + l * 768, ln1_b + l * 768, XB, 0, qb,
-        nullptr, nullptr, t, 0, nullptr, nullptr, nullptr, nullptr);
-      cross_attn_k<<<dim3(RR, 12), 64, 0, stream>>>(
-          qb, ck + (size_t)l * 4 * 128 * 768, cv + (size_t)l * 4 * 128 * 768, source_mask, attnb);
-      G(coT[l], cross_out_w + (size_t)l * 768 * 768, 768, cross_out_b + l * 768, 768,
-        0, attnb, nullptr, nullptr, nullptr, nullptr, 0, tmp,
-        nullptr, nullptr, t, 0, nullptr, nullptr, nullptr, nullptr);
-      G(f1T[l], ff1_w + (size_t)l * 3072 * 768, 3072, ff1_b + l * 3072, 3072,
-        2, XB, tmp, ln2_g + l * 768, ln2_b + l * 768, XC, 1, ffb,
-        nullptr, nullptr, t, 0, nullptr, nullptr, nullptr, nullptr);
-      if (useWT) ff2_k<true><<<48, 1024, 0, stream>>>(f2T[l], ff2_b + l * 768, ffb, tmp);
-      else       ff2_k<false><<<48, 1024, 0, stream>>>(ff2_w + (size_t)l * 768 * 3072, ff2_b + l * 768, ffb, tmp);
-    }
-    G(dT, dense_w, 768, dense_b, 768,
-      2, XC, tmp, ln3_g + 768, ln3_b + 768, nullptr, 2, hbuf,
-      nullptr, nullptr, t, 0, nullptr, nullptr, nullptr, nullptr);
-    if (useET) logits_k<true><<<LB, 256, 0, stream>>>(hbuf, embT, candV, candI, mrow, srow);
-    else       logits_k<false><<<LB, 256, 0, stream>>>(hbuf, emb, candV, candI, mrow, srow);
-    topk_k<<<BB, 256, 0, stream>>>(candV, candI, mrow, srow, scores, bc, bn, t, prevKp, tokp);
-  }
-
-  finalize_k<<<1, 64, 0, stream>>>(scores, bufs0, (float*)d_out);
-}
+  DecP P;
+  P.emb = emb; P.pos = pos; P.ln_emb_g = ln_emb_g; P.ln_emb_b = ln_emb_b;
+  P.self_in_b = self_in_b; P.self_out_b = self_out_b;
+  P.cross_in_b = cross_in_b; P.cross_out_b = cross_out_b;
+  P.ff1_b = ff1_b; P.ff2_b = ff2_b; P.dense_b = dense_b;
+  P.ln1_g = ln1_g; P.ln1_b = ln1_b; P.ln2_g = ln2_g; P.ln2_b = ln2_b;
+  P.ln3_g = ln3_g; P.ln3_b = ln3_b;
+  P.smask = source_mask;
+  if (useWT) {
+    P.Wqkv0 = siT[0]; P.Wqkv1 = siT[1]; P.Wso0 = soT[0]; P.Wso1 = soT[1];
+    P.Wcq0 = ciT[0]; P.Wcq1 = ciT[1]; P.Wco0 = coT[0]; P.Wco1 = coT[1];
+    P.Wf10 = f1T[0]; P.Wf11 = f1T[1]; P.Wf20 = f2T[0]; P.Wf21 = f2T[1];
+    P.Wd = dT; P.embM = useET ? embT : emb;
+  } else {
+    P.Wqkv0 = self_in_w; P.Wqkv1 = self_in_w + (size_t)2304 * 768;
+    P.Wso0 = self_out_w; P.Wso1 = self_out_w + (size_t)768 * 768;
+    P.Wcq0 = cross_in_w; P.Wcq1 = cross_in_w + (size_t)2304 * 768;
+    P.Wco0 = cross_out_w; P.Wco1 = cross_out_w + (size_t)768 * 768;
+    P.Wf10 = ff1_w; P.Wf11 = ff1_w + (size_t)3072 * 768;
+    P.Wf20 = ff2_w; P.Wf21 = ff2_w + (size_t)768 * 3072;
+    P.Wd = dense_w; P.embM = emb;
+  }
+  P.XA = XA; P.XB = XB; P.XC = XC; P.qb = qb; P.attnb = attnb; P.tmp = tmp;
+  P.hbuf = hbuf; P.ffb = ffb; P.pf = pf;
+  P.candV = candV; P.mrow = mrow; P.srow = srow; P.scores = scores;
+  P.ck = ck; P.cv = cv; P.kcB = kcB; P.vcB = vcB;
+  P.candI = candI; P.bufs0 = bufs0; P.bufs1 = bufs1; P.prevK = prevKp; P.tok = tokp;
+  P.bar = bar; P.out = (float*)d_out;
+
+  if (useET)      decode_k<true,  true ><<<NBLK, 256, 0, stream>>>(P);
+  else if (useWT) decode_k<true,  false><<<NBLK, 256, 0, stream>>>(P);
+  else            decode_k<false, false><<<NBLK, 256, 0, stream>>>(P);
+}
```
